# Performance work log

Measured on AMD Instinct MI355X. Metric: run time of the kernel, lower is better.

## Reference

```python
import jax, jax.numpy as jnp
import numpy as np

N_NODES = 50000
N_EDGES = 800000
D_IN = 128
D_OUT = 128


def setup_inputs() -> dict:
    key = jax.random.key(0)
    k_x, k_r, k_c, k_v, k_w = jax.random.split(key, 5)
    x = jax.random.normal(k_x, (N_NODES, D_IN), dtype=jnp.float32)
    edge_row = jax.random.randint(k_r, (N_EDGES,), 0, N_NODES)  # destination nodes
    edge_col = jax.random.randint(k_c, (N_EDGES,), 0, N_NODES)  # source nodes
    edge_val = jax.random.uniform(k_v, (N_EDGES,), dtype=jnp.float32)
    W = jax.random.normal(k_w, (D_OUT, D_IN), dtype=jnp.float32) * (1.0 / np.sqrt(D_IN))
    bias = jnp.zeros((D_OUT,), dtype=jnp.float32)
    return {"x": x, "edge_row": edge_row, "edge_col": edge_col,
            "edge_val": edge_val, "W": W, "bias": bias}


def reference(x, edge_row, edge_col, edge_val, W, bias):
    # support = linear(x)   (nn.Linear with bias=False: x @ W.T)
    support = jnp.einsum('ni,oi->no', x, W)  # [N, D_OUT]
    # out = sparse.mm(adj, support): gather source rows, scale by edge value,
    # scatter-add into destination rows.
    msgs = edge_val[:, None] * support[edge_col]  # [E, D_OUT]
    out = jax.ops.segment_sum(msgs, edge_row, num_segments=N_NODES)
    return out + bias
```

## Files before the change

kernel.cpp:

```cpp
#include <hip/hip_runtime.h>
#include <hip/hip_bf16.h>


constexpr int D     = 128;
constexpr int NPB   = 64;
constexpr int CAP   = 2048;
constexpr int C1    = 3200;
constexpr int BT    = 1024;
constexpr int NBMAX = 1024;

__device__ inline unsigned int bf1(float f) {
    unsigned int u = __float_as_uint(f);
    return (u + 0x7fffu + ((u >> 16) & 1u)) >> 16;
}
__device__ inline unsigned int cvt2(float a, float b) {
    __hip_bfloat162 h = __float22bfloat162_rn(float2{a, b});
    return *reinterpret_cast<unsigned int*>(&h);
}
__device__ inline float bflo(unsigned int u) { return __uint_as_float(u << 16); }
__device__ inline float bfhi(unsigned int u) { return __uint_as_float(u & 0xffff0000u); }

__global__ __launch_bounds__(256) void cvt_bf16_kernel(const float* __restrict__ in,
                                                       uint4* __restrict__ out, int n8,
                                                       int* __restrict__ gcursor, int nb) {
    int i = blockIdx.x * 256 + threadIdx.x;
    if (i < nb) gcursor[i] = 0;
    if (i >= n8) return;
    const float4* p = (const float4*)in + (size_t)i * 2;
    float4 a = p[0], b = p[1];
    uint4 r;
    r.x = cvt2(a.x, a.y); r.y = cvt2(a.z, a.w);
    r.z = cvt2(b.x, b.y); r.w = cvt2(b.z, b.w);
    out[i] = r;
}

__global__ __launch_bounds__(256) void gemm_mfma_kernel(const float* __restrict__ x,
                                                        const unsigned short* __restrict__ Wb,
                                                        unsigned short* __restrict__ supb,
                                                        int n_nodes) {
    using frag  = __attribute__((ext_vector_type(8))) short;
    using f32x4 = __attribute__((ext_vector_type(4))) float;
    union FU { uint4 u; frag f; };
    const int wv = threadIdx.x >> 6;
    const int lane = threadIdx.x & 63;
    const int m = lane & 15, quad = lane >> 4;
    const int row0 = blockIdx.x * 128 + wv * 32;
    const bool full = (row0 + 32 <= n_nodes);
    const int r0 = full ? row0 + m      : min(row0 + m, n_nodes - 1);
    const int r1 = full ? row0 + 16 + m : min(row0 + 16 + m, n_nodes - 1);

    frag a0[4], a1[4];
#pragma unroll
    for (int kf = 0; kf < 4; ++kf) {
        const float4* xp0 = (const float4*)(x + (size_t)r0 * D + kf * 32 + quad * 8);
        float4 p = xp0[0], q = xp0[1];
        FU t;
        t.u.x = cvt2(p.x, p.y); t.u.y = cvt2(p.z, p.w);
        t.u.z = cvt2(q.x, q.y); t.u.w = cvt2(q.z, q.w);
        a0[kf] = t.f;
        const float4* xp1 = (const float4*)(x + (size_t)r1 * D + kf * 32 + quad * 8);
        p = xp1[0]; q = xp1[1];
        t.u.x = cvt2(p.x, p.y); t.u.y = cvt2(p.z, p.w);
        t.u.z = cvt2(q.x, q.y); t.u.w = cvt2(q.z, q.w);
        a1[kf] = t.f;
    }

    f32x4 acc0[8], acc1[8];
#pragma unroll
    for (int ct = 0; ct < 8; ++ct) {
        acc0[ct] = (f32x4){0.f, 0.f, 0.f, 0.f};
        acc1[ct] = (f32x4){0.f, 0.f, 0.f, 0.f};
    }

#pragma unroll
    for (int ct = 0; ct < 8; ++ct) {
        const unsigned short* wrow = Wb + (size_t)(ct * 16 + m) * D;
#pragma unroll
        for (int kf = 0; kf < 4; ++kf) {
            frag b = *(const frag*)(wrow + kf * 32 + quad * 8);
            acc0[ct] = __builtin_amdgcn_mfma_f32_16x16x32_bf16(a0[kf], b, acc0[ct], 0, 0, 0);
            acc1[ct] = __builtin_amdgcn_mfma_f32_16x16x32_bf16(a1[kf], b, acc1[ct], 0, 0, 0);
        }
    }

    if (full) {
#pragma unroll
        for (int ct = 0; ct < 8; ++ct) {
#pragma unroll
            for (int r = 0; r < 4; ++r) {
                int rr0 = row0 + quad * 4 + r;
                supb[(size_t)rr0 * D + ct * 16 + m] = (unsigned short)bf1(acc0[ct][r]);
                supb[(size_t)(rr0 + 16) * D + ct * 16 + m] = (unsigned short)bf1(acc1[ct][r]);
            }
        }
    } else {
#pragma unroll
        for (int ct = 0; ct < 8; ++ct) {
#pragma unroll
            for (int r = 0; r < 4; ++r) {
                int rr0 = row0 + quad * 4 + r;
                if (rr0 < n_nodes)
                    supb[(size_t)rr0 * D + ct * 16 + m] = (unsigned short)bf1(acc0[ct][r]);
                int rr1 = rr0 + 16;
                if (rr1 < n_nodes)
                    supb[(size_t)rr1 * D + ct * 16 + m] = (unsigned short)bf1(acc1[ct][r]);
            }
        }
    }
}

__global__ __launch_bounds__(BT) void binpass_kernel(const int* __restrict__ erow,
                                                     const int* __restrict__ ecol,
                                                     const float* __restrict__ eval,
                                                     int* __restrict__ gcursor,
                                                     int2* __restrict__ coarse,
                                                     int n_edges, int nb) {
    __shared__ int bkcnt[NBMAX];
    __shared__ int bkoff[NBMAX];
    __shared__ int wsum[16];
    __shared__ int gbase[NBMAX];
    __shared__ unsigned short slotbk[C1];
    __shared__ int2 stage[C1];
    const int t = threadIdx.x;
    const int base = blockIdx.x * C1;
    const int m = min(C1, n_edges - base);

    for (int i = t; i < nb; i += BT) bkcnt[i] = 0;
    __syncthreads();

    constexpr int EPT = (C1 + BT - 1) / BT;
    int  bk[EPT], rank[EPT];
    int2 pk[EPT];
#pragma unroll
    for (int j = 0; j < EPT; ++j) {
        int i = t + j * BT;
        bk[j] = -1;
        if (i < m) {
            int e = base + i;
            int dst = erow[e];
            int b = dst / NPB;
            bk[j] = b;
            rank[j] = atomicAdd(&bkcnt[b], 1);
            pk[j] = make_int2(ecol[e] | ((dst & (NPB - 1)) << 20),
                              __float_as_int(eval[e]));
        }
    }
    __syncthreads();

    {
        const int w = t >> 6, l = t & 63;
        int v = (t < nb) ? bkcnt[t] : 0;
        int inc = v;
#pragma unroll
        for (int o = 1; o < 64; o <<= 1) {
            int u = __shfl_up(inc, o, 64);
            if (l >= o) inc += u;
        }
        if (l == 63) wsum[w] = inc;
        __syncthreads();
        if (t < 16) {
            int wv2 = wsum[t];
            int winc = wv2;
#pragma unroll
            for (int o = 1; o < 16; o <<= 1) {
                int u = __shfl_up(winc, o, 16);
                if (t >= o) winc += u;
            }
            wsum[t] = winc - wv2;
        }
        __syncthreads();
        if (t < nb) bkoff[t] = inc - v + wsum[w];
    }
    __syncthreads();

#pragma unroll
    for (int j = 0; j < EPT; ++j) {
        if (bk[j] >= 0) {
            int s = bkoff[bk[j]] + rank[j];
            stage[s] = pk[j];
            slotbk[s] = (unsigned short)bk[j];
        }
    }
    if (t < nb) {
        int c = bkcnt[t];
        gbase[t] = (c > 0) ? (t * CAP + atomicAdd(&gcursor[t], c)) : 0;
    }
    __syncthreads();

    for (int i = t; i < m; i += BT) {
        int b = slotbk[i];
        int p = gbase[b] + (i - bkoff[b]);
        if (p < (b + 1) * CAP) coarse[p] = stage[i];
    }
}

__global__ __launch_bounds__(BT) void sortgather_kernel(const int* __restrict__ gcursor,
                                                        const int2* __restrict__ coarse,
                                                        const unsigned short* __restrict__ supb,
                                                        const float* __restrict__ bias,
                                                        float* __restrict__ out,
                                                        int n_nodes) {
    __shared__ int ncnt[NPB];
    __shared__ int noff[NPB];
    __shared__ int ncur[NPB];
    __shared__ int2 sorted[CAP];
    const int t = threadIdx.x;
    const int b = blockIdx.x;
    const int node0 = b * NPB;
    const int m = min(gcursor[b], CAP);
    const int2* src = coarse + (size_t)b * CAP;

    if (t < NPB) ncnt[t] = 0;
    __syncthreads();

    constexpr int EPT2 = CAP / BT;
    int2 ee[EPT2];
    int  dl[EPT2];
#pragma unroll
    for (int j = 0; j < EPT2; ++j) {
        int i = t + j * BT;
        dl[j] = -1;
        if (i < m) {
            ee[j] = src[i];
            dl[j] = (ee[j].x >> 20) & (NPB - 1);
            atomicAdd(&ncnt[dl[j]], 1);
        }
    }
    __syncthreads();

    if (t < NPB) {
        int v = ncnt[t];
        int inc = v;
        for (int o = 1; o < NPB; o <<= 1) {
            int u = __shfl_up(inc, o, 64);
            if (t >= o) inc += u;
        }
        noff[t] = inc - v;
        ncur[t] = inc - v;
    }
    __syncthreads();

#pragma unroll
    for (int j = 0; j < EPT2; ++j) {
        if (dl[j] >= 0) {
            int p = atomicAdd(&ncur[dl[j]], 1);
            sorted[p] = make_int2(ee[j].x & 0xFFFFF, ee[j].y);
        }
    }
    __syncthreads();

    const int qw = t >> 4;
    const int l16 = t & 15;
    const int node = node0 + qw;
    if (node >= n_nodes) return;
    const int beg = noff[qw];
    const int end = beg + ncnt[qw];

    const float4* b4 = (const float4*)(bias + l16 * 8);
    float4 acc0 = b4[0], acc1 = b4[1];

    int e = beg;
    for (; e + 3 < end; e += 4) {
        int2 d0 = sorted[e], d1 = sorted[e + 1], d2 = sorted[e + 2], d3 = sorted[e + 3];
        uint4 u0 = *(const uint4*)(supb + (size_t)d0.x * D + l16 * 8);
        uint4 u1 = *(const uint4*)(supb + (size_t)d1.x * D + l16 * 8);
        uint4 u2 = *(const uint4*)(supb + (size_t)d2.x * D + l16 * 8);
        uint4 u3 = *(const uint4*)(supb + (size_t)d3.x * D + l16 * 8);
        float v0 = __int_as_float(d0.y), v1 = __int_as_float(d1.y);
        float v2 = __int_as_float(d2.y), v3 = __int_as_float(d3.y);
        acc0.x += v0 * bflo(u0.x) + v1 * bflo(u1.x) + v2 * bflo(u2.x) + v3 * bflo(u3.x);
        acc0.y += v0 * bfhi(u0.x) + v1 * bfhi(u1.x) + v2 * bfhi(u2.x) + v3 * bfhi(u3.x);
        acc0.z += v0 * bflo(u0.y) + v1 * bflo(u1.y) + v2 * bflo(u2.y) + v3 * bflo(u3.y);
        acc0.w += v0 * bfhi(u0.y) + v1 * bfhi(u1.y) + v2 * bfhi(u2.y) + v3 * bfhi(u3.y);
        acc1.x += v0 * bflo(u0.z) + v1 * bflo(u1.z) + v2 * bflo(u2.z) + v3 * bflo(u3.z);
        acc1.y += v0 * bfhi(u0.z) + v1 * bfhi(u1.z) + v2 * bfhi(u2.z) + v3 * bfhi(u3.z);
        acc1.z += v0 * bflo(u0.w) + v1 * bflo(u1.w) + v2 * bflo(u2.w) + v3 * bflo(u3.w);
        acc1.w += v0 * bfhi(u0.w) + v1 * bfhi(u1.w) + v2 * bfhi(u2.w) + v3 * bfhi(u3.w);
    }
    for (; e < end; ++e) {
        int2 d0 = sorted[e];
        uint4 u0 = *(const uint4*)(supb + (size_t)d0.x * D + l16 * 8);
        float v0 = __int_as_float(d0.y);
        acc0.x += v0 * bflo(u0.x); acc0.y += v0 * bfhi(u0.x);
        acc0.z += v0 * bflo(u0.y); acc0.w += v0 * bfhi(u0.y);
        acc1.x += v0 * bflo(u0.z); acc1.y += v0 * bfhi(u0.z);
        acc1.z += v0 * bflo(u0.w); acc1.w += v0 * bfhi(u0.w);
    }
    float4* o4 = (float4*)(out + (size_t)node * D + l16 * 8);
    o4[0] = acc0;
    o4[1] = acc1;
}

__global__ __launch_bounds__(256) void init_out_kernel(float4* __restrict__ out4,
                                                       const float4* __restrict__ bias4,
                                                       int total4) {
    int i = blockIdx.x * 256 + threadIdx.x;
    if (i < total4) out4[i] = bias4[i & 31];
}

__global__ __launch_bounds__(256) void scatter_fb_kernel(const int* __restrict__ erow,
                                                         const int* __restrict__ ecol,
                                                         const float* __restrict__ eval,
                                                         const unsigned short* __restrict__ supb,
                                                         float* __restrict__ out,
                                                         int n_edges) {
    int e = blockIdx.x * 8 + (threadIdx.x >> 5);
    if (e >= n_edges) return;
    int lane = threadIdx.x & 31;
    int src = ecol[e], dst = erow[e];
    float v = eval[e];
    const unsigned short* sp = supb + (size_t)src * D + lane * 4;
    float* op = out + (size_t)dst * D + lane * 4;
#pragma unroll
    for (int j = 0; j < 4; ++j)
        atomicAdd(op + j, v * __uint_as_float(((unsigned)sp[j]) << 16));
}

static inline size_t align_up(size_t v, size_t a) { return (v + a - 1) & ~(a - 1); }

extern "C" void kernel_launch(void* const* d_in, const int* in_sizes, int n_in,
                              void* d_out, int out_size, void* d_ws, size_t ws_size,
                              hipStream_t stream) {
    const float* x    = (const float*)d_in[0];
    const int*   erow = (const int*)d_in[1];
    const int*   ecol = (const int*)d_in[2];
    const float* eval = (const float*)d_in[3];
    const float* W    = (const float*)d_in[4];
    const float* bias = (const float*)d_in[5];
    float* out = (float*)d_out;

    const int n_nodes = in_sizes[0] / D;
    const int n_edges = in_sizes[1];
    const int nb = (n_nodes + NPB - 1) / NPB;

    char* base = (char*)d_ws;
    size_t off = 0;
    unsigned short* supb = (unsigned short*)(base + off); off = align_up(off + (size_t)n_nodes * D * 2, 256);
    unsigned short* Wb   = (unsigned short*)(base + off); off = align_up(off + (size_t)D * D * 2, 256);
    int*  gcursor = (int*)(base + off);  off = align_up(off + (size_t)nb * 4, 256);
    int2* coarse  = (int2*)(base + off); off = align_up(off + (size_t)nb * CAP * 8, 256);

    const int n8 = D * D / 8;
    const int cvt_grid = (max(n8, nb) + 255) / 256;
    const bool fast = (n_nodes < (1 << 20)) && (nb <= NBMAX) && (off <= ws_size);

    cvt_bf16_kernel<<<cvt_grid, 256, 0, stream>>>(W, (uint4*)Wb, n8, gcursor, fast ? nb : 0);
    gemm_mfma_kernel<<<(n_nodes + 127) / 128, 256, 0, stream>>>(x, Wb, supb, n_nodes);

    if (fast) {
        binpass_kernel<<<(n_edges + C1 - 1) / C1, BT, 0, stream>>>(
            erow, ecol, eval, gcursor, coarse, n_edges, nb);
        sortgather_kernel<<<nb, BT, 0, stream>>>(
            gcursor, coarse, supb, bias, out, n_nodes);
    } else {
        int total4 = n_nodes * (D / 4);
        init_out_kernel<<<(total4 + 255) / 256, 256, 0, stream>>>(
            (float4*)out, (const float4*)bias, total4);
        scatter_fb_kernel<<<(n_edges + 7) / 8, 256, 0, stream>>>(
            erow, ecol, eval, supb, out, n_edges);
    }
}
```

Baseline: 142.7 us.

## Fuse GEMM and edge binning into one heterogeneous kernel launch

Merges the dense bf16 MFMA GEMM and the edge bin pass into a single launch. Blocks below nbin bin edges and the remaining blocks compute support rows, so the two independent stages can overlap on the GPU and one launch boundary goes away. GEMM blocks now use 1024 threads covering 512 rows, with accumulators scoped per column tile to reduce register pressure. The cost is that GEMM blocks carry the binning kernel's large shared-memory footprint, which may lower occupancy.

Measured after the change: 154.5 us. 8.3% more time.

```diff
diff --git a/kernel.cpp b/kernel.cpp
--- a/kernel.cpp
+++ b/kernel.cpp
@@ -8,6 +8,7 @@
 constexpr int C1    = 3200;
 constexpr int BT    = 1024;
 constexpr int NBMAX = 1024;
+constexpr int GRPB  = 512;
 
 __device__ inline unsigned int bf1(float f) {
     unsigned int u = __float_as_uint(f);
@@ -34,163 +35,152 @@
     out[i] = r;
 }
 
-__global__ __launch_bounds__(256) void gemm_mfma_kernel(const float* __restrict__ x,
-                                                        const unsigned short* __restrict__ Wb,
-                                                        unsigned short* __restrict__ supb,
-                                                        int n_nodes) {
-    using frag  = __attribute__((ext_vector_type(8))) short;
-    using f32x4 = __attribute__((ext_vector_type(4))) float;
-    union FU { uint4 u; frag f; };
-    const int wv = threadIdx.x >> 6;
-    const int lane = threadIdx.x & 63;
-    const int m = lane & 15, quad = lane >> 4;
-    const int row0 = blockIdx.x * 128 + wv * 32;
-    const bool full = (row0 + 32 <= n_nodes);
-    const int r0 = full ? row0 + m      : min(row0 + m, n_nodes - 1);
-    const int r1 = full ? row0 + 16 + m : min(row0 + 16 + m, n_nodes - 1);
-
-    frag a0[4], a1[4];
-#pragma unroll
-    for (int kf = 0; kf < 4; ++kf) {
-        const float4* xp0 = (const float4*)(x + (size_t)r0 * D + kf * 32 + quad * 8);
-        float4 p = xp0[0], q = xp0[1];
-        FU t;
-        t.u.x = cvt2(p.x, p.y); t.u.y = cvt2(p.z, p.w);
-        t.u.z = cvt2(q.x, q.y); t.u.w = cvt2(q.z, q.w);
-        a0[kf] = t.f;
-        const float4* xp1 = (const float4*)(x + (size_t)r1 * D + kf * 32 + quad * 8);
-        p = xp1[0]; q = xp1[1];
-        t.u.x = cvt2(p.x, p.y); t.u.y = cvt2(p.z, p.w);
-        t.u.z = cvt2(q.x, q.y); t.u.w = cvt2(q.z, q.w);
-        a1[kf] = t.f;
-    }
-
-    f32x4 acc0[8], acc1[8];
-#pragma unroll
-    for (int ct = 0; ct < 8; ++ct) {
-        acc0[ct] = (f32x4){0.f, 0.f, 0.f, 0.f};
-        acc1[ct] = (f32x4){0.f, 0.f, 0.f, 0.f};
-    }
-
-#pragma unroll
-    for (int ct = 0; ct < 8; ++ct) {
-        const unsigned short* wrow = Wb + (size_t)(ct * 16 + m) * D;
-#pragma unroll
-        for (int kf = 0; kf < 4; ++kf) {
-            frag b = *(const frag*)(wrow + kf * 32 + quad * 8);
-            acc0[ct] = __builtin_amdgcn_mfma_f32_16x16x32_bf16(a0[kf], b, acc0[ct], 0, 0, 0);
-            acc1[ct] = __builtin_amdgcn_mfma_f32_16x16x32_bf16(a1[kf], b, acc1[ct], 0, 0, 0);
-        }
-    }
-
-    if (full) {
-#pragma unroll
-        for (int ct = 0; ct < 8; ++ct) {
-#pragma unroll
-            for (int r = 0; r < 4; ++r) {
-                int rr0 = row0 + quad * 4 + r;
-                supb[(size_t)rr0 * D + ct * 16 + m] = (unsigned short)bf1(acc0[ct][r]);
-                supb[(size_t)(rr0 + 16) * D + ct * 16 + m] = (unsigned short)bf1(acc1[ct][r]);
-            }
-        }
-    } else {
-#pragma unroll
-        for (int ct = 0; ct < 8; ++ct) {
-#pragma unroll
-            for (int r = 0; r < 4; ++r) {
-                int rr0 = row0 + quad * 4 + r;
-                if (rr0 < n_nodes)
-                    supb[(size_t)rr0 * D + ct * 16 + m] = (unsigned short)bf1(acc0[ct][r]);
-                int rr1 = rr0 + 16;
-                if (rr1 < n_nodes)
-                    supb[(size_t)rr1 * D + ct * 16 + m] = (unsigned short)bf1(acc1[ct][r]);
-            }
-        }
-    }
-}
-
-__global__ __launch_bounds__(BT) void binpass_kernel(const int* __restrict__ erow,
-                                                     const int* __restrict__ ecol,
-                                                     const float* __restrict__ eval,
-                                                     int* __restrict__ gcursor,
-                                                     int2* __restrict__ coarse,
-                                                     int n_edges, int nb) {
+__global__ __launch_bounds__(BT) void gemm_binpass_kernel(
+        const float* __restrict__ x, const unsigned short* __restrict__ Wb,
+        unsigned short* __restrict__ supb, int n_nodes,
+        const int* __restrict__ erow, const int* __restrict__ ecol,
+        const float* __restrict__ eval, int* __restrict__ gcursor,
+        int2* __restrict__ coarse, int n_edges, int nb, int nbin) {
     __shared__ int bkcnt[NBMAX];
     __shared__ int bkoff[NBMAX];
     __shared__ int wsum[16];
     __shared__ int gbase[NBMAX];
     __shared__ unsigned short slotbk[C1];
     __shared__ int2 stage[C1];
+
     const int t = threadIdx.x;
-    const int base = blockIdx.x * C1;
-    const int m = min(C1, n_edges - base);
-
-    for (int i = t; i < nb; i += BT) bkcnt[i] = 0;
-    __syncthreads();
-
-    constexpr int EPT = (C1 + BT - 1) / BT;
-    int  bk[EPT], rank[EPT];
-    int2 pk[EPT];
-#pragma unroll
-    for (int j = 0; j < EPT; ++j) {
-        int i = t + j * BT;
-        bk[j] = -1;
-        if (i < m) {
-            int e = base + i;
-            int dst = erow[e];
-            int b = dst / NPB;
-            bk[j] = b;
-            rank[j] = atomicAdd(&bkcnt[b], 1);
-            pk[j] = make_int2(ecol[e] | ((dst & (NPB - 1)) << 20),
-                              __float_as_int(eval[e]));
-        }
-    }
-    __syncthreads();
-
-    {
-        const int w = t >> 6, l = t & 63;
-        int v = (t < nb) ? bkcnt[t] : 0;
-        int inc = v;
-#pragma unroll
-        for (int o = 1; o < 64; o <<= 1) {
-            int u = __shfl_up(inc, o, 64);
-            if (l >= o) inc += u;
-        }
-        if (l == 63) wsum[w] = inc;
+
+    if ((int)blockIdx.x < nbin) {
+        const int base = blockIdx.x * C1;
+        const int m = min(C1, n_edges - base);
+
+        for (int i = t; i < nb; i += BT) bkcnt[i] = 0;
         __syncthreads();
-        if (t < 16) {
-            int wv2 = wsum[t];
-            int winc = wv2;
-#pragma unroll
-            for (int o = 1; o < 16; o <<= 1) {
-                int u = __shfl_up(winc, o, 16);
-                if (t >= o) winc += u;
-            }
-            wsum[t] = winc - wv2;
+
+        constexpr int EPT = (C1 + BT - 1) / BT;
+        int  bk[EPT], rank[EPT];
+        int2 pk[EPT];
+#pragma unroll
+        for (int j = 0; j < EPT; ++j) {
+            int i = t + j * BT;
+            bk[j] = -1;
+            if (i < m) {
+                int e = base + i;
+                int dst = erow[e];
+                int b = dst / NPB;
+                bk[j] = b;
+                rank[j] = atomicAdd(&bkcnt[b], 1);
+                pk[j] = make_int2(ecol[e] | ((dst & (NPB - 1)) << 20),
+                                  __float_as_int(eval[e]));
+            }
         }
         __syncthreads();
-        if (t < nb) bkoff[t] = inc - v + wsum[w];
-    }
-    __syncthreads();
-
-#pragma unroll
-    for (int j = 0; j < EPT; ++j) {
-        if (bk[j] >= 0) {
-            int s = bkoff[bk[j]] + rank[j];
-            stage[s] = pk[j];
-            slotbk[s] = (unsigned short)bk[j];
-        }
-    }
-    if (t < nb) {
-        int c = bkcnt[t];
-        gbase[t] = (c > 0) ? (t * CAP + atomicAdd(&gcursor[t], c)) : 0;
-    }
-    __syncthreads();
-
-    for (int i = t; i < m; i += BT) {
-        int b = slotbk[i];
-        int p = gbase[b] + (i - bkoff[b]);
-        if (p < (b + 1) * CAP) coarse[p] = stage[i];
+
+        {
+            const int w = t >> 6, l = t & 63;
+            int v = (t < nb) ? bkcnt[t] : 0;
+            int inc = v;
+#pragma unroll
+            for (int o = 1; o < 64; o <<= 1) {
+                int u = __shfl_up(inc, o, 64);
+                if (l >= o) inc += u;
+            }
+            if (l == 63) wsum[w] = inc;
+            __syncthreads();
+            if (t < 16) {
+                int wv2 = wsum[t];
+                int winc = wv2;
+#pragma unroll
+                for (int o = 1; o < 16; o <<= 1) {
+                    int u = __shfl_up(winc, o, 16);
+                    if (t >= o) winc += u;
+                }
+                wsum[t] = winc - wv2;
+            }
+            __syncthreads();
+            if (t < nb) bkoff[t] = inc - v + wsum[w];
+        }
+        __syncthreads();
+
+#pragma unroll
+        for (int j = 0; j < EPT; ++j) {
+            if (bk[j] >= 0) {
+                int s = bkoff[bk[j]] + rank[j];
+                stage[s] = pk[j];
+                slotbk[s] = (unsigned short)bk[j];
+            }
+        }
+        if (t < nb) {
+            int c = bkcnt[t];
+            gbase[t] = (c > 0) ? (t * CAP + atomicAdd(&gcursor[t], c)) : 0;
+        }
+        __syncthreads();
+
+        for (int i = t; i < m; i += BT) {
+            int b = slotbk[i];
+            int p = gbase[b] + (i - bkoff[b]);
+            if (p < (b + 1) * CAP) coarse[p] = stage[i];
+        }
+        return;
+    }
+
+    using frag  = __attribute__((ext_vector_type(8))) short;
+    using f32x4 = __attribute__((ext_vector_type(4))) float;
+    union FU { uint4 u; frag f; };
+    const int gblk = blockIdx.x - nbin;
+    const int wv = t >> 6;
+    const int lane = t & 63;
+    const int m = lane & 15, quad = lane >> 4;
+    const int row0 = gblk * GRPB + wv * 32;
+    const bool full = (row0 + 32 <= n_nodes);
+    const int r0 = full ? row0 + m      : min(row0 + m, n_nodes - 1);
+    const int r1 = full ? row0 + 16 + m : min(row0 + 16 + m, n_nodes - 1);
+
+    frag a0[4], a1[4];
+#pragma unroll
+    for (int kf = 0; kf < 4; ++kf) {
+        const float4* xp0 = (const float4*)(x + (size_t)r0 * D + kf * 32 + quad * 8);
+        float4 p = xp0[0], q = xp0[1];
+        FU tt;
+        tt.u.x = cvt2(p.x, p.y); tt.u.y = cvt2(p.z, p.w);
+        tt.u.z = cvt2(q.x, q.y); tt.u.w = cvt2(q.z, q.w);
+        a0[kf] = tt.f;
+        const float4* xp1 = (const float4*)(x + (size_t)r1 * D + kf * 32 + quad * 8);
+        p = xp1[0]; q = xp1[1];
+        tt.u.x = cvt2(p.x, p.y); tt.u.y = cvt2(p.z, p.w);
+        tt.u.z = cvt2(q.x, q.y); tt.u.w = cvt2(q.z, q.w);
+        a1[kf] = tt.f;
+    }
+
+#pragma unroll
+    for (int ct = 0; ct < 8; ++ct) {
+        f32x4 acc0 = (f32x4){0.f, 0.f, 0.f, 0.f};
+        f32x4 acc1 = (f32x4){0.f, 0.f, 0.f, 0.f};
+        const unsigned short* wrow = Wb + (size_t)(ct * 16 + m) * D;
+#pragma unroll
+        for (int kf = 0; kf < 4; ++kf) {
+            frag b = *(const frag*)(wrow + kf * 32 + quad * 8);
+            acc0 = __builtin_amdgcn_mfma_f32_16x16x32_bf16(a0[kf], b, acc0, 0, 0, 0);
+            acc1 = __builtin_amdgcn_mfma_f32_16x16x32_bf16(a1[kf], b, acc1, 0, 0, 0);
+        }
+        if (full) {
+#pragma unroll
+            for (int r = 0; r < 4; ++r) {
+                int rr0 = row0 + quad * 4 + r;
+                supb[(size_t)rr0 * D + ct * 16 + m] = (unsigned short)bf1(acc0[r]);
+                supb[(size_t)(rr0 + 16) * D + ct * 16 + m] = (unsigned short)bf1(acc1[r]);
+            }
+        } else {
+#pragma unroll
+            for (int r = 0; r < 4; ++r) {
+                int rr0 = row0 + quad * 4 + r;
+                if (rr0 < n_nodes)
+                    supb[(size_t)rr0 * D + ct * 16 + m] = (unsigned short)bf1(acc0[r]);
+                int rr1 = rr0 + 16;
+                if (rr1 < n_nodes)
+                    supb[(size_t)rr1 * D + ct * 16 + m] = (unsigned short)bf1(acc1[r]);
+            }
+        }
     }
 }
 
@@ -344,12 +334,15 @@
     const int cvt_grid = (max(n8, nb) + 255) / 256;
     const bool fast = (n_nodes < (1 << 20)) && (nb <= NBMAX) && (off <= ws_size);
 
+    const int nbin  = fast ? (n_edges + C1 - 1) / C1 : 0;
+    const int ngemm = (n_nodes + GRPB - 1) / GRPB;
+
     cvt_bf16_kernel<<<cvt_grid, 256, 0, stream>>>(W, (uint4*)Wb, n8, gcursor, fast ? nb : 0);
-    gemm_mfma_kernel<<<(n_nodes + 127) / 128, 256, 0, stream>>>(x, Wb, supb, n_nodes);
+
+    gemm_binpass_kernel<<<nbin + ngemm, BT, 0, stream>>>(
+        x, Wb, supb, n_nodes, erow, ecol, eval, gcursor, coarse, n_edges, nb, nbin);
 
     if (fast) {
-        binpass_kernel<<<(n_edges + C1 - 1) / C1, BT, 0, stream>>>(
-            erow, ecol, eval, gcursor, coarse, n_edges, nb);
         sortgather_kernel<<<nb, BT, 0, stream>>>(
             gcursor, coarse, supb, bias, out, n_nodes);
     } else {
```
